# Kernel tuning notes

Hardware: AMD Instinct MI355X
Metric: run time of the kernel (lower is better)

The kernel has to match this reference:

```python
import jax, jax.numpy as jnp
import numpy as np

N = 50000
E = 600000
IN_C = 128
HID = 128
OUT_C = 2


def setup_inputs() -> dict:
    key = jax.random.key(0)
    ks = jax.random.split(key, 16)
    x = jax.random.normal(ks[0], (N, IN_C), dtype=jnp.float32)
    edge_index = jax.random.randint(ks[1], (2, E), 0, N, dtype=jnp.int64)
    s = 0.05
    # policy_net: Linear(2*in, 64) -> ReLU -> Linear(64, 1) -> Sigmoid
    W_p1 = jax.random.normal(ks[2], (64, 2 * IN_C), dtype=jnp.float32) * s
    b_p1 = jnp.zeros((64,), dtype=jnp.float32)
    W_p2 = jax.random.normal(ks[3], (1, 64), dtype=jnp.float32) * s
    b_p2 = jnp.zeros((1,), dtype=jnp.float32)
    # GCNConv weights (lin without bias + separate bias, PyG convention)
    W1 = jax.random.normal(ks[4], (HID, IN_C), dtype=jnp.float32) * s
    b1 = jnp.zeros((HID,), dtype=jnp.float32)
    W2 = jax.random.normal(ks[5], (HID, HID), dtype=jnp.float32) * s
    b2 = jnp.zeros((HID,), dtype=jnp.float32)
    W_lin = jax.random.normal(ks[6], (OUT_C, HID), dtype=jnp.float32) * s
    b_lin = jnp.zeros((OUT_C,), dtype=jnp.float32)
    return {"x": x, "edge_index": edge_index, "W_p1": W_p1, "b_p1": b_p1,
            "W_p2": W_p2, "b_p2": b_p2, "W1": W1, "b1": b1, "W2": W2,
            "b2": b2, "W_lin": W_lin, "b_lin": b_lin}


def gcn_conv(x, src, dst, edge_weight, W, b, n_nodes):
    # PyG GCNConv with normalize=True, add_self_loops=True, given edge_weight.
    loop = jnp.arange(n_nodes, dtype=src.dtype)
    s = jnp.concatenate([src, loop])
    d = jnp.concatenate([dst, loop])
    w = jnp.concatenate([edge_weight, jnp.ones((n_nodes,), x.dtype)])
    deg = jax.ops.segment_sum(w, d, num_segments=n_nodes)
    dinv = jnp.where(deg > 0, jax.lax.rsqrt(jnp.where(deg > 0, deg, 1.0)), 0.0)
    norm = dinv[s] * w * dinv[d]  # [E+N]
    xl = x @ W.T  # [N, out]
    msg = norm[:, None] * xl[s]  # gather + scale
    agg = jax.ops.segment_sum(msg, d, num_segments=n_nodes)
    return agg + b


def reference(x, edge_index, W_p1, b_p1, W_p2, b_p2, W1, b1, W2, b2, W_lin, b_lin):
    src, dst = edge_index[0], edge_index[1]
    # edge-weight policy MLP on gathered, concatenated endpoint features
    cat_feat = jnp.concatenate([x[src], x[dst]], axis=1)  # [E, 2*in]
    h = jax.nn.relu(cat_feat @ W_p1.T + b_p1)
    edge_weight = jax.nn.sigmoid(h @ W_p2.T + b_p2)[:, 0]  # [E]
    x1 = jax.nn.relu(gcn_conv(x, src, dst, edge_weight, W1, b1, N))
    x2 = jax.nn.relu(gcn_conv(x1, src, dst, edge_weight, W2, b2, N))
    out = x2 @ W_lin.T + b_lin
    return jax.nn.sigmoid(out)
```

## Files before the change

### kernel.cpp

```cpp
#include <hip/hip_runtime.h>
#include <hip/hip_bf16.h>

#define NN 50000
#define NE 600000
#define CPAD 16

typedef __attribute__((ext_vector_type(8))) short short8;
typedef __attribute__((ext_vector_type(8))) _Float16 half8;
typedef __attribute__((ext_vector_type(4))) float floatx4;

__device__ __forceinline__ short bf16_bits(float v) {
    __hip_bfloat16 h = __float2bfloat16(v);
    return *reinterpret_cast<short*>(&h);
}

__global__ void k_init_cvt(const int* __restrict__ raw, int* __restrict__ count,
                           int* __restrict__ flag, const float* __restrict__ wp1,
                           const float* __restrict__ w1, const float* __restrict__ w2,
                           __hip_bfloat16* __restrict__ wcatb, __hip_bfloat16* __restrict__ w1b,
                           __hip_bfloat16* __restrict__ w2b) {
    int i = blockIdx.x * blockDim.x + threadIdx.x;
    if (i < NN) {
        count[(size_t)i * CPAD] = 0;
    }
    if (i < 16384) {
        int r = i >> 7, c = i & 127;
        float v = (r < 64) ? wp1[r * 256 + c] : wp1[(r - 64) * 256 + 128 + c];
        wcatb[i] = __float2bfloat16(v);
    } else if (i < 32768) {
        w1b[i - 16384] = __float2bfloat16(w1[i - 16384]);
    } else if (i < 49152) {
        w2b[i - 32768] = __float2bfloat16(w2[i - 32768]);
    }
    if (blockIdx.x == 0) {
        if (threadIdx.x == 0) *flag = 0;
        __syncthreads();
        int any = 0;
        for (int j = threadIdx.x; j < 1024; j += 256) any |= raw[2 * j + 1];
        if (any) atomicOr(flag, 1);
    }
}

#define GG 782
__global__ __launch_bounds__(256) void k_uv_count(
    const float* __restrict__ x, const __hip_bfloat16* __restrict__ Wb,
    const float* __restrict__ bp1, _Float16* __restrict__ uvh,
    __hip_bfloat16* __restrict__ xb, const int* __restrict__ raw,
    const int* __restrict__ flag, int* __restrict__ count, int* __restrict__ rank) {
    if (blockIdx.x >= GG) {
        int e = (blockIdx.x - GG) * blockDim.x + threadIdx.x;
        if (e < NE) {
            int d = (*flag) ? raw[NE + e] : (int)((const long long*)raw)[NE + e];
            rank[e] = atomicAdd(&count[(size_t)d * CPAD], 1);
        }
        return;
    }
    const int lane = threadIdx.x & 63;
    const int wave = threadIdx.x >> 6;
    const int col = lane & 15;
    const int quad = lane >> 4;

    short8 bfrag[4][8];
    const short* wp = (const short*)Wb;
#pragma unroll
    for (int tt = 0; tt < 8; ++tt) {
        int row = tt * 16 + col;
#pragma unroll
        for (int kk = 0; kk < 4; ++kk)
            bfrag[kk][tt] = *(const short8*)(wp + row * 128 + kk * 32 + quad * 8);
    }
    int tile = blockIdx.x * 4 + wave;
    if (tile >= NN / 16) return;
    int base = tile * 16;

    floatx4 acc[8];
#pragma unroll
    for (int t = 0; t < 8; ++t) acc[t] = (floatx4){0.f, 0.f, 0.f, 0.f};
#pragma unroll
    for (int kk = 0; kk < 4; ++kk) {
        const float* xrow = x + (size_t)(base + col) * 128 + kk * 32 + quad * 8;
        float4 f0 = ((const float4*)xrow)[0];
        float4 f1 = ((const float4*)xrow)[1];
        short8 afrag;
        afrag[0] = bf16_bits(f0.x); afrag[1] = bf16_bits(f0.y);
        afrag[2] = bf16_bits(f0.z); afrag[3] = bf16_bits(f0.w);
        afrag[4] = bf16_bits(f1.x); afrag[5] = bf16_bits(f1.y);
        afrag[6] = bf16_bits(f1.z); afrag[7] = bf16_bits(f1.w);
        *(short8*)((short*)xb + (size_t)(base + col) * 128 + kk * 32 + quad * 8) = afrag;
#pragma unroll
        for (int tt = 0; tt < 8; ++tt)
            acc[tt] = __builtin_amdgcn_mfma_f32_16x16x32_bf16(afrag, bfrag[kk][tt], acc[tt], 0, 0, 0);
    }
#pragma unroll
    for (int tt = 0; tt < 8; ++tt) {
        int n = tt * 16 + col;
        float badd = (tt >= 4) ? bp1[n - 64] : 0.f;
#pragma unroll
        for (int r = 0; r < 4; ++r) {
            int row = base + quad * 4 + r;
            uvh[(size_t)row * 128 + n] = (_Float16)(acc[tt][r] + badd);
        }
    }
}

__global__ void k_scan_block(const int* __restrict__ count, int* __restrict__ tmp,
                             int* __restrict__ bsums) {
    __shared__ int s[512];
    int tid = threadIdx.x;
    int i = blockIdx.x * 512 + tid;
    s[tid] = (i < NN) ? count[(size_t)i * CPAD] : 0;
    __syncthreads();
    for (int off = 1; off < 512; off <<= 1) {
        int t = (tid >= off) ? s[tid - off] : 0;
        __syncthreads();
        s[tid] += t;
        __syncthreads();
    }
    if (i < NN) tmp[i] = s[tid];
    if (tid == 511) bsums[blockIdx.x] = s[511];
}

__global__ void k_finalize(const int* __restrict__ tmp, const int* __restrict__ bsums,
                           int* __restrict__ rowptr) {
    __shared__ int sb[128];
    int tid = threadIdx.x;
    if (tid < 128) sb[tid] = (tid < 98) ? bsums[tid] : 0;
    __syncthreads();
    for (int off = 1; off < 128; off <<= 1) {
        int t = (tid < 128 && tid >= off) ? sb[tid - off] : 0;
        __syncthreads();
        if (tid < 128) sb[tid] += t;
        __syncthreads();
    }
    int i = blockIdx.x * blockDim.x + tid;
    if (i >= NN) return;
    int blk = i >> 9;
    int add = blk ? sb[blk - 1] : 0;
    int incl = tmp[i] + add;
    rowptr[i + 1] = incl;
    if (i == 0) rowptr[0] = 0;
}

__global__ void k_fill(const int* __restrict__ raw, const int* __restrict__ flag,
                       const int* __restrict__ rank, const int* __restrict__ rowptr,
                       int2* __restrict__ meta) {
    int e = blockIdx.x * blockDim.x + threadIdx.x;
    if (e >= NE) return;
    int s, d;
    if (*flag) {
        s = raw[e];
        d = raw[NE + e];
    } else {
        const long long* r64 = (const long long*)raw;
        s = (int)r64[e];
        d = (int)r64[NE + e];
    }
    int pos = rowptr[d] + rank[e];
    meta[pos] = make_int2(s, 0);
}

__global__ __launch_bounds__(256) void k_policy_csr(
    const _Float16* __restrict__ uvh, const float* __restrict__ wp2,
    const float* __restrict__ bp2, const int* __restrict__ rowptr,
    int2* __restrict__ meta, float* __restrict__ deg) {
    int wid = (blockIdx.x * blockDim.x + threadIdx.x) >> 6;
    int lane = threadIdx.x & 63;
    if (wid >= NN) return;
    int g = lane >> 3, c = lane & 7;
    half8 vh = *(const half8*)(uvh + (size_t)wid * 128 + 64 + c * 8);
    float vv[8], w2v[8];
    const float4* w2p = (const float4*)(wp2 + c * 8);
    float4 wa = w2p[0], wb = w2p[1];
    w2v[0] = wa.x; w2v[1] = wa.y; w2v[2] = wa.z; w2v[3] = wa.w;
    w2v[4] = wb.x; w2v[5] = wb.y; w2v[6] = wb.z; w2v[7] = wb.w;
#pragma unroll
    for (int j = 0; j < 8; ++j) vv[j] = (float)vh[j];
    float b2 = bp2[0];
    int beg = rowptr[wid], end = rowptr[wid + 1];
    float degsum = 0.f;
    int p = beg + g;
    for (; p + 8 < end; p += 16) {
        int s1 = meta[p].x, s2 = meta[p + 8].x;
        half8 u1 = *(const half8*)(uvh + (size_t)s1 * 128 + c * 8);
        half8 u2 = *(const half8*)(uvh + (size_t)s2 * 128 + c * 8);
        float p1 = 0.f, p2 = 0.f;
#pragma unroll
        for (int j = 0; j < 8; ++j) {
            float h1 = (float)u1[j] + vv[j];
            float h2 = (float)u2[j] + vv[j];
            h1 = h1 > 0.f ? h1 : 0.f;
            h2 = h2 > 0.f ? h2 : 0.f;
            p1 += h1 * w2v[j];
            p2 += h2 * w2v[j];
        }
        p1 += __shfl_xor(p1, 1, 64); p2 += __shfl_xor(p2, 1, 64);
        p1 += __shfl_xor(p1, 2, 64); p2 += __shfl_xor(p2, 2, 64);
        p1 += __shfl_xor(p1, 4, 64); p2 += __shfl_xor(p2, 4, 64);
        if (c == 0) {
            float e1 = 1.f / (1.f + __expf(-(p1 + b2)));
            float e2 = 1.f / (1.f + __expf(-(p2 + b2)));
            meta[p].y = __float_as_int(e1);
            meta[p + 8].y = __float_as_int(e2);
            degsum += e1 + e2;
        }
    }
    if (p < end) {
        int s1 = meta[p].x;
        half8 u1 = *(const half8*)(uvh + (size_t)s1 * 128 + c * 8);
        float p1 = 0.f;
#pragma unroll
        for (int j = 0; j < 8; ++j) {
            float h1 = (float)u1[j] + vv[j];
            h1 = h1 > 0.f ? h1 : 0.f;
            p1 += h1 * w2v[j];
        }
        p1 += __shfl_xor(p1, 1, 64);
        p1 += __shfl_xor(p1, 2, 64);
        p1 += __shfl_xor(p1, 4, 64);
        if (c == 0) {
            float e1 = 1.f / (1.f + __expf(-(p1 + b2)));
            meta[p].y = __float_as_int(e1);
            degsum += e1;
        }
    }
    degsum += __shfl_xor(degsum, 8, 64);
    degsum += __shfl_xor(degsum, 16, 64);
    degsum += __shfl_xor(degsum, 32, 64);
    if (lane == 0) deg[wid] = 1.f + degsum;
}

__global__ __launch_bounds__(256) void k_gemm(
    const __hip_bfloat16* __restrict__ A, const __hip_bfloat16* __restrict__ Wb,
    const float* __restrict__ deg, _Float16* __restrict__ xlh) {
    const int lane = threadIdx.x & 63;
    const int wave = threadIdx.x >> 6;
    const int col = lane & 15;
    const int quad = lane >> 4;

    short8 bfrag[4][8];
    const short* wp = (const short*)Wb;
#pragma unroll
    for (int tt = 0; tt < 8; ++tt) {
        int row = tt * 16 + col;
#pragma unroll
        for (int kk = 0; kk < 4; ++kk)
            bfrag[kk][tt] = *(const short8*)(wp + row * 128 + kk * 32 + quad * 8);
    }
    int tile = blockIdx.x * 4 + wave;
    if (tile >= NN / 16) return;
    int base = tile * 16;
    const short* xs = (const short*)A;

    floatx4 acc[8];
#pragma unroll
    for (int t = 0; t < 8; ++t) acc[t] = (floatx4){0.f, 0.f, 0.f, 0.f};
#pragma unroll
    for (int kk = 0; kk < 4; ++kk) {
        short8 afrag = *(const short8*)(xs + (size_t)(base + col) * 128 + kk * 32 + quad * 8);
#pragma unroll
        for (int tt = 0; tt < 8; ++tt)
            acc[tt] = __builtin_amdgcn_mfma_f32_16x16x32_bf16(afrag, bfrag[kk][tt], acc[tt], 0, 0, 0);
    }
    float di[4];
#pragma unroll
    for (int r = 0; r < 4; ++r) di[r] = rsqrtf(deg[base + quad * 4 + r]);
#pragma unroll
    for (int tt = 0; tt < 8; ++tt) {
        int n = tt * 16 + col;
#pragma unroll
        for (int r = 0; r < 4; ++r) {
            int row = base + quad * 4 + r;
            xlh[(size_t)row * 128 + n] = (_Float16)(di[r] * acc[tt][r]);
        }
    }
}

__device__ __forceinline__ void scatter_core(
    const int* __restrict__ rowptr, const int2* __restrict__ meta,
    const _Float16* __restrict__ xlh, int wid, int g, int c, float acc[8]) {
    int beg = rowptr[wid], end = rowptr[wid + 1];
    int p = beg + g;
    for (; p + 12 < end; p += 16) {
        int2 m1 = meta[p], m2 = meta[p + 4], m3 = meta[p + 8], m4 = meta[p + 12];
        half8 r1 = *(const half8*)(xlh + (size_t)m1.x * 128 + c * 8);
        half8 r2 = *(const half8*)(xlh + (size_t)m2.x * 128 + c * 8);
        half8 r3 = *(const half8*)(xlh + (size_t)m3.x * 128 + c * 8);
        half8 r4 = *(const half8*)(xlh + (size_t)m4.x * 128 + c * 8);
        float c1 = __int_as_float(m1.y), c2 = __int_as_float(m2.y);
        float c3 = __int_as_float(m3.y), c4 = __int_as_float(m4.y);
#pragma unroll
        for (int j = 0; j < 8; ++j)
            acc[j] += c1 * (float)r1[j] + c2 * (float)r2[j] + c3 * (float)r3[j] + c4 * (float)r4[j];
    }
    for (; p + 4 < end; p += 8) {
        int2 m1 = meta[p], m2 = meta[p + 4];
        half8 r1 = *(const half8*)(xlh + (size_t)m1.x * 128 + c * 8);
        half8 r2 = *(const half8*)(xlh + (size_t)m2.x * 128 + c * 8);
        float c1 = __int_as_float(m1.y), c2 = __int_as_float(m2.y);
#pragma unroll
        for (int j = 0; j < 8; ++j) acc[j] += c1 * (float)r1[j] + c2 * (float)r2[j];
    }
    if (p < end) {
        int2 m1 = meta[p];
        half8 r1 = *(const half8*)(xlh + (size_t)m1.x * 128 + c * 8);
        float c1 = __int_as_float(m1.y);
#pragma unroll
        for (int j = 0; j < 8; ++j) acc[j] += c1 * (float)r1[j];
    }
#pragma unroll
    for (int j = 0; j < 8; ++j) {
        acc[j] += __shfl_xor(acc[j], 16, 64);
        acc[j] += __shfl_xor(acc[j], 32, 64);
    }
}

__global__ __launch_bounds__(256) void k_scatter_mid(
    const int* __restrict__ rowptr, const int2* __restrict__ meta,
    const float* __restrict__ deg, const _Float16* __restrict__ xlh,
    const float* __restrict__ bias, __hip_bfloat16* __restrict__ xb2) {
    int wid = (blockIdx.x * blockDim.x + threadIdx.x) >> 6;
    int lane = threadIdx.x & 63;
    if (wid >= NN) return;
    int g = lane >> 4, c = lane & 15;
    float acc[8] = {0.f, 0.f, 0.f, 0.f, 0.f, 0.f, 0.f, 0.f};
    scatter_core(rowptr, meta, xlh, wid, g, c, acc);
    if (g == 0) {
        float dn = rsqrtf(deg[wid]);
        half8 sv = *(const half8*)(xlh + (size_t)wid * 128 + c * 8);
        const float4* bp = (const float4*)(bias + c * 8);
        float4 ba = bp[0], bb = bp[1];
        float bv[8] = {ba.x, ba.y, ba.z, ba.w, bb.x, bb.y, bb.z, bb.w};
        short8 o;
#pragma unroll
        for (int j = 0; j < 8; ++j) {
            float t = bv[j] + dn * ((float)sv[j] + acc[j]);
            t = t > 0.f ? t : 0.f;
            o[j] = bf16_bits(t);
        }
        *(short8*)((short*)xb2 + (size_t)wid * 128 + c * 8) = o;
    }
}

__global__ __launch_bounds__(256) void k_scatter_out(
    const int* __restrict__ rowptr, const int2* __restrict__ meta,
    const float* __restrict__ deg, const _Float16* __restrict__ xlh,
    const float* __restrict__ bias, const float* __restrict__ wlin,
    const float* __restrict__ blin, float* __restrict__ out) {
    int wid = (blockIdx.x * blockDim.x + threadIdx.x) >> 6;
    int lane = threadIdx.x & 63;
    if (wid >= NN) return;
    int g = lane >> 4, c = lane & 15;
    float acc[8] = {0.f, 0.f, 0.f, 0.f, 0.f, 0.f, 0.f, 0.f};
    scatter_core(rowptr, meta, xlh, wid, g, c, acc);
    if (g == 0) {
        float dn = rsqrtf(deg[wid]);
        half8 sv = *(const half8*)(xlh + (size_t)wid * 128 + c * 8);
        const float4* bp = (const float4*)(bias + c * 8);
        float4 ba = bp[0], bb = bp[1];
        float bv[8] = {ba.x, ba.y, ba.z, ba.w, bb.x, bb.y, bb.z, bb.w};
        float p0 = 0.f, p1 = 0.f;
#pragma unroll
        for (int j = 0; j < 8; ++j) {
            float t = bv[j] + dn * ((float)sv[j] + acc[j]);
            t = t > 0.f ? t : 0.f;
            p0 += t * wlin[c * 8 + j];
            p1 += t * wlin[128 + c * 8 + j];
        }
#pragma unroll
        for (int off = 1; off < 16; off <<= 1) {
            p0 += __shfl_xor(p0, off, 64);
            p1 += __shfl_xor(p1, off, 64);
        }
        if (c == 0) {
            out[wid * 2 + 0] = 1.f / (1.f + __expf(-(p0 + blin[0])));
            out[wid * 2 + 1] = 1.f / (1.f + __expf(-(p1 + blin[1])));
        }
    }
}


extern "C" void kernel_launch(void* const* d_in, const int* in_sizes, int n_in,
                              void* d_out, int out_size, void* d_ws, size_t ws_size,
                              hipStream_t stream) {
    const float* x = (const float*)d_in[0];
    const int* eidx_raw = (const int*)d_in[1];
    const float* W_p1 = (const float*)d_in[2];
    const float* b_p1 = (const float*)d_in[3];
    const float* W_p2 = (const float*)d_in[4];
    const float* b_p2 = (const float*)d_in[5];
    const float* W1 = (const float*)d_in[6];
    const float* b1 = (const float*)d_in[7];
    const float* W2 = (const float*)d_in[8];
    const float* b2 = (const float*)d_in[9];
    const float* W_lin = (const float*)d_in[10];
    const float* b_lin = (const float*)d_in[11];
    float* out = (float*)d_out;

    char* ws = (char*)d_ws;
    size_t off = 0;
    auto alloc = [&](size_t bytes) -> void* {
        off = (off + 255) & ~(size_t)255;
        void* p = ws + off;
        off += bytes;
        return p;
    };
    float* deg = (float*)alloc(NN * 4);
    int* rowptr = (int*)alloc((NN + 1) * 4);
    int* count = (int*)alloc((size_t)NN * CPAD * 4);
    int* flag = (int*)alloc(4);
    int* bsums = (int*)alloc(128 * 4);
    int* rank = (int*)alloc((size_t)NE * 4);
    int2* meta = (int2*)alloc((size_t)NE * 8);
    __hip_bfloat16* xb = (__hip_bfloat16*)alloc((size_t)NN * 128 * 2);
    _Float16* xlh = (_Float16*)alloc((size_t)NN * 128 * 2);
    _Float16* uvh = (_Float16*)alloc((size_t)NN * 128 * 2);
    __hip_bfloat16* wcatb = (__hip_bfloat16*)alloc(128 * 128 * 2);
    __hip_bfloat16* w1b = (__hip_bfloat16*)alloc(128 * 128 * 2);
    __hip_bfloat16* w2b = (__hip_bfloat16*)alloc(128 * 128 * 2);
    int* tmp = (int*)meta;

    const int TB = 256;
    int gN = (NN + TB - 1) / TB;
    int gE = (NE + TB - 1) / TB;
    int gS = (NN + 3) / 4;

    k_init_cvt<<<gN, TB, 0, stream>>>(eidx_raw, count, flag, W_p1, W1, W2, wcatb, w1b, w2b);
    k_uv_count<<<GG + gE, TB, 0, stream>>>(x, wcatb, b_p1, uvh, xb, eidx_raw, flag, count, rank);

    k_scan_block<<<98, 512, 0, stream>>>(count, tmp, bsums);
    k_finalize<<<gN, TB, 0, stream>>>(tmp, bsums, rowptr);
    k_fill<<<gE, TB, 0, stream>>>(eidx_raw, flag, rank, rowptr, meta);

    k_policy_csr<<<gS, TB, 0, stream>>>(uvh, W_p2, b_p2, rowptr, meta, deg);

    k_gemm<<<GG, TB, 0, stream>>>(xb, w1b, deg, xlh);
    k_scatter_mid<<<gS, TB, 0, stream>>>(rowptr, meta, deg, xlh, b1, xb);
    k_gemm<<<GG, TB, 0, stream>>>(xb, w2b, deg, xlh);
    k_scatter_out<<<gS, TB, 0, stream>>>(rowptr, meta, deg, xlh, b2, W_lin, b_lin, out);
}
```

Baseline: 272.8 us.

## Compute edge policy in edge order alongside degree counting, then fill CSR

Moves the edge-weight policy MLP out of the CSR-ordered per-node kernel into an edge-ordered kernel that shares a launch with the atomic degree counting, so the policy work overlaps the count atomics. Weights go to a flat per-edge buffer and are copied into the CSR meta array during fill. A small kernel then sums the weights per node to get the degree. In exchange there is an extra launch, an extra NE-sized float buffer, and each edge now gathers its destination's v-row instead of reusing a per-node register copy.

```diff
diff --git a/kernel.cpp b/kernel.cpp
--- a/kernel.cpp
+++ b/kernel.cpp
@@ -42,19 +42,10 @@
 }
 
 #define GG 782
-__global__ __launch_bounds__(256) void k_uv_count(
+__global__ __launch_bounds__(256) void k_uv(
     const float* __restrict__ x, const __hip_bfloat16* __restrict__ Wb,
     const float* __restrict__ bp1, _Float16* __restrict__ uvh,
-    __hip_bfloat16* __restrict__ xb, const int* __restrict__ raw,
-    const int* __restrict__ flag, int* __restrict__ count, int* __restrict__ rank) {
-    if (blockIdx.x >= GG) {
-        int e = (blockIdx.x - GG) * blockDim.x + threadIdx.x;
-        if (e < NE) {
-            int d = (*flag) ? raw[NE + e] : (int)((const long long*)raw)[NE + e];
-            rank[e] = atomicAdd(&count[(size_t)d * CPAD], 1);
-        }
-        return;
-    }
+    __hip_bfloat16* __restrict__ xb) {
     const int lane = threadIdx.x & 63;
     const int wave = threadIdx.x >> 6;
     const int col = lane & 15;
@@ -100,6 +91,65 @@
             int row = base + quad * 4 + r;
             uvh[(size_t)row * 128 + n] = (_Float16)(acc[tt][r] + badd);
         }
+    }
+}
+
+#define GCNT 256
+#define GPOL 9375
+__global__ __launch_bounds__(256) void k_cnt_policy(
+    const int* __restrict__ raw, const int* __restrict__ flag,
+    int* __restrict__ count, int* __restrict__ rank,
+    const _Float16* __restrict__ uvh, const float* __restrict__ wp2,
+    const float* __restrict__ bp2, float* __restrict__ ew_flat) {
+    const bool f32 = (*flag) != 0;
+    const long long* r64 = (const long long*)raw;
+    if (blockIdx.x < GCNT) {
+        int tid = blockIdx.x * 256 + threadIdx.x;
+        for (int e = tid; e < NE; e += GCNT * 256) {
+            int d = f32 ? raw[NE + e] : (int)r64[NE + e];
+            rank[e] = atomicAdd(&count[(size_t)d * CPAD], 1);
+        }
+        return;
+    }
+    int pb = blockIdx.x - GCNT;
+    int wave = threadIdx.x >> 6, lane = threadIdx.x & 63;
+    int g = lane >> 3, c = lane & 7;
+    int e1 = pb * 64 + wave * 16 + g;
+    int e2 = e1 + 8;
+    int s1, d1, s2, d2;
+    if (f32) {
+        s1 = raw[e1]; d1 = raw[NE + e1];
+        s2 = raw[e2]; d2 = raw[NE + e2];
+    } else {
+        s1 = (int)r64[e1]; d1 = (int)r64[NE + e1];
+        s2 = (int)r64[e2]; d2 = (int)r64[NE + e2];
+    }
+    half8 u1 = *(const half8*)(uvh + (size_t)s1 * 128 + c * 8);
+    half8 v1 = *(const half8*)(uvh + (size_t)d1 * 128 + 64 + c * 8);
+    half8 u2 = *(const half8*)(uvh + (size_t)s2 * 128 + c * 8);
+    half8 v2 = *(const half8*)(uvh + (size_t)d2 * 128 + 64 + c * 8);
+    float w2v[8];
+    const float4* w2p = (const float4*)(wp2 + c * 8);
+    float4 wa = w2p[0], wb = w2p[1];
+    w2v[0] = wa.x; w2v[1] = wa.y; w2v[2] = wa.z; w2v[3] = wa.w;
+    w2v[4] = wb.x; w2v[5] = wb.y; w2v[6] = wb.z; w2v[7] = wb.w;
+    float b2 = bp2[0];
+    float p1 = 0.f, p2 = 0.f;
+#pragma unroll
+    for (int j = 0; j < 8; ++j) {
+        float h1 = (float)u1[j] + (float)v1[j];
+        float h2 = (float)u2[j] + (float)v2[j];
+        h1 = h1 > 0.f ? h1 : 0.f;
+        h2 = h2 > 0.f ? h2 : 0.f;
+        p1 += h1 * w2v[j];
+        p2 += h2 * w2v[j];
+    }
+    p1 += __shfl_xor(p1, 1, 64); p2 += __shfl_xor(p2, 1, 64);
+    p1 += __shfl_xor(p1, 2, 64); p2 += __shfl_xor(p2, 2, 64);
+    p1 += __shfl_xor(p1, 4, 64); p2 += __shfl_xor(p2, 4, 64);
+    if (c == 0) {
+        ew_flat[e1] = 1.f / (1.f + __expf(-(p1 + b2)));
+        ew_flat[e2] = 1.f / (1.f + __expf(-(p2 + b2)));
     }
 }
 
@@ -143,7 +193,7 @@
 
 __global__ void k_fill(const int* __restrict__ raw, const int* __restrict__ flag,
                        const int* __restrict__ rank, const int* __restrict__ rowptr,
-                       int2* __restrict__ meta) {
+                       const float* __restrict__ ew_flat, int2* __restrict__ meta) {
     int e = blockIdx.x * blockDim.x + threadIdx.x;
     if (e >= NE) return;
     int s, d;
@@ -156,77 +206,21 @@
         d = (int)r64[NE + e];
     }
     int pos = rowptr[d] + rank[e];
-    meta[pos] = make_int2(s, 0);
-}
-
-__global__ __launch_bounds__(256) void k_policy_csr(
-    const _Float16* __restrict__ uvh, const float* __restrict__ wp2,
-    const float* __restrict__ bp2, const int* __restrict__ rowptr,
-    int2* __restrict__ meta, float* __restrict__ deg) {
+    meta[pos] = make_int2(s, __float_as_int(ew_flat[e]));
+}
+
+__global__ __launch_bounds__(256) void k_deg(const int* __restrict__ rowptr,
+                                             const int2* __restrict__ meta,
+                                             float* __restrict__ deg) {
     int wid = (blockIdx.x * blockDim.x + threadIdx.x) >> 6;
     int lane = threadIdx.x & 63;
     if (wid >= NN) return;
-    int g = lane >> 3, c = lane & 7;
-    half8 vh = *(const half8*)(uvh + (size_t)wid * 128 + 64 + c * 8);
-    float vv[8], w2v[8];
-    const float4* w2p = (const float4*)(wp2 + c * 8);
-    float4 wa = w2p[0], wb = w2p[1];
-    w2v[0] = wa.x; w2v[1] = wa.y; w2v[2] = wa.z; w2v[3] = wa.w;
-    w2v[4] = wb.x; w2v[5] = wb.y; w2v[6] = wb.z; w2v[7] = wb.w;
-#pragma unroll
-    for (int j = 0; j < 8; ++j) vv[j] = (float)vh[j];
-    float b2 = bp2[0];
     int beg = rowptr[wid], end = rowptr[wid + 1];
-    float degsum = 0.f;
-    int p = beg + g;
-    for (; p + 8 < end; p += 16) {
-        int s1 = meta[p].x, s2 = meta[p + 8].x;
-        half8 u1 = *(const half8*)(uvh + (size_t)s1 * 128 + c * 8);
-        half8 u2 = *(const half8*)(uvh + (size_t)s2 * 128 + c * 8);
-        float p1 = 0.f, p2 = 0.f;
-#pragma unroll
-        for (int j = 0; j < 8; ++j) {
-            float h1 = (float)u1[j] + vv[j];
-            float h2 = (float)u2[j] + vv[j];
-            h1 = h1 > 0.f ? h1 : 0.f;
-            h2 = h2 > 0.f ? h2 : 0.f;
-            p1 += h1 * w2v[j];
-            p2 += h2 * w2v[j];
-        }
-        p1 += __shfl_xor(p1, 1, 64); p2 += __shfl_xor(p2, 1, 64);
-        p1 += __shfl_xor(p1, 2, 64); p2 += __shfl_xor(p2, 2, 64);
-        p1 += __shfl_xor(p1, 4, 64); p2 += __shfl_xor(p2, 4, 64);
-        if (c == 0) {
-            float e1 = 1.f / (1.f + __expf(-(p1 + b2)));
-            float e2 = 1.f / (1.f + __expf(-(p2 + b2)));
-            meta[p].y = __float_as_int(e1);
-            meta[p + 8].y = __float_as_int(e2);
-            degsum += e1 + e2;
-        }
-    }
-    if (p < end) {
-        int s1 = meta[p].x;
-        half8 u1 = *(const half8*)(uvh + (size_t)s1 * 128 + c * 8);
-        float p1 = 0.f;
-#pragma unroll
-        for (int j = 0; j < 8; ++j) {
-            float h1 = (float)u1[j] + vv[j];
-            h1 = h1 > 0.f ? h1 : 0.f;
-            p1 += h1 * w2v[j];
-        }
-        p1 += __shfl_xor(p1, 1, 64);
-        p1 += __shfl_xor(p1, 2, 64);
-        p1 += __shfl_xor(p1, 4, 64);
-        if (c == 0) {
-            float e1 = 1.f / (1.f + __expf(-(p1 + b2)));
-            meta[p].y = __float_as_int(e1);
-            degsum += e1;
-        }
-    }
-    degsum += __shfl_xor(degsum, 8, 64);
-    degsum += __shfl_xor(degsum, 16, 64);
-    degsum += __shfl_xor(degsum, 32, 64);
-    if (lane == 0) deg[wid] = 1.f + degsum;
+    float s = 0.f;
+    for (int p = beg + lane; p < end; p += 64) s += __int_as_float(meta[p].y);
+#pragma unroll
+    for (int off = 1; off < 64; off <<= 1) s += __shfl_xor(s, off, 64);
+    if (lane == 0) deg[wid] = 1.f + s;
 }
 
 __global__ __launch_bounds__(256) void k_gemm(
@@ -410,6 +404,7 @@
     int* flag = (int*)alloc(4);
     int* bsums = (int*)alloc(128 * 4);
     int* rank = (int*)alloc((size_t)NE * 4);
+    float* ew_flat = (float*)alloc((size_t)NE * 4);
     int2* meta = (int2*)alloc((size_t)NE * 8);
     __hip_bfloat16* xb = (__hip_bfloat16*)alloc((size_t)NN * 128 * 2);
     _Float16* xlh = (_Float16*)alloc((size_t)NN * 128 * 2);
@@ -425,13 +420,13 @@
     int gS = (NN + 3) / 4;
 
     k_init_cvt<<<gN, TB, 0, stream>>>(eidx_raw, count, flag, W_p1, W1, W2, wcatb, w1b, w2b);
-    k_uv_count<<<GG + gE, TB, 0, stream>>>(x, wcatb, b_p1, uvh, xb, eidx_raw, flag, count, rank);
+    k_uv<<<GG, TB, 0, stream>>>(x, wcatb, b_p1, uvh, xb);
+    k_cnt_policy<<<GCNT + GPOL, TB, 0, stream>>>(eidx_raw, flag, count, rank, uvh, W_p2, b_p2, ew_flat);
 
     k_scan_block<<<98, 512, 0, stream>>>(count, tmp, bsums);
     k_finalize<<<gN, TB, 0, stream>>>(tmp, bsums, rowptr);
-    k_fill<<<gE, TB, 0, stream>>>(eidx_raw, flag, rank, rowptr, meta);
-
-    k_policy_csr<<<gS, TB, 0, stream>>>(uvh, W_p2, b_p2, rowptr, meta, deg);
+    k_fill<<<gE, TB, 0, stream>>>(eidx_raw, flag, rank, rowptr, ew_flat, meta);
+    k_deg<<<gS, TB, 0, stream>>>(rowptr, meta, deg);
 
     k_gemm<<<GG, TB, 0, stream>>>(xb, w1b, deg, xlh);
     k_scatter_mid<<<gS, TB, 0, stream>>>(rowptr, meta, deg, xlh, b1, xb);
```

Result: no change. 277.5 us (+1.7%).
